# Optimization experiments

Hardware: AMD Instinct MI355X
Metric: run time of the kernel (lower is better)

## Reference

```python
import jax, jax.numpy as jnp
import numpy as np

N_NODES = 100000


def gcn_conv(x, edge_index, W, b, add_self_loops=True):
    """PyG GCNConv: out = D^{-1/2}(A+I)D^{-1/2} (x @ W) + b, sum-aggregated at col."""
    n = x.shape[0]
    x = x @ W  # linear first, like PyG (smaller feature dim usually)
    row, col = edge_index[0], edge_index[1]
    if add_self_loops:
        loop = jnp.arange(n, dtype=row.dtype)
        row = jnp.concatenate([row, loop])
        col = jnp.concatenate([col, loop])
    ones = jnp.ones(row.shape[0], dtype=x.dtype)
    deg = jax.ops.segment_sum(ones, col, num_segments=n)  # in-degree incl. self loops
    dinv = jnp.where(deg > 0, jax.lax.rsqrt(deg), 0.0)
    norm = dinv[row] * dinv[col]  # [E]
    msg = x[row] * norm[:, None]  # gather + scale, [E, F]
    out = jax.ops.segment_sum(msg, col, num_segments=n)  # scatter-add
    return out + b


def setup_inputs() -> dict:
    key = jax.random.key(0)
    ks = jax.random.split(key, 12)
    latent_dim, condition_dim, hidden_dim, output_dim = 64, 32, 64, 64
    n_edges = 1600000
    latent = jax.random.normal(ks[0], (N_NODES, latent_dim), dtype=jnp.float32)
    condition = jax.random.normal(ks[1], (N_NODES, condition_dim), dtype=jnp.float32)
    edge_index = jax.random.randint(ks[2], (2, n_edges), 0, N_NODES, dtype=jnp.int64 if jax.config.jax_enable_x64 else jnp.int32)

    def glorot(k, fan_in, fan_out):
        s = jnp.sqrt(6.0 / (fan_in + fan_out))
        return jax.random.uniform(k, (fan_in, fan_out), minval=-s, maxval=s, dtype=jnp.float32)

    W1 = glorot(ks[3], latent_dim, hidden_dim); b1 = jnp.zeros((hidden_dim,), jnp.float32)
    W2 = glorot(ks[4], condition_dim, hidden_dim); b2 = jnp.zeros((hidden_dim,), jnp.float32)
    W3 = glorot(ks[5], 2 * hidden_dim, hidden_dim); b3 = jnp.zeros((hidden_dim,), jnp.float32)
    W4 = glorot(ks[6], hidden_dim, output_dim); b4 = jnp.zeros((output_dim,), jnp.float32)
    return {"latent": latent, "condition": condition, "edge_index": edge_index,
            "W1": W1, "b1": b1, "W2": W2, "b2": b2,
            "W3": W3, "b3": b3, "W4": W4, "b4": b4}


def reference(latent, condition, edge_index, W1, b1, W2, b2, W3, b3, W4, b4):
    z2h = gcn_conv(latent, edge_index, W1, b1)
    c2h = gcn_conv(condition, edge_index, W2, b2)
    h = jnp.concatenate([z2h, c2h], axis=1)
    h = gcn_conv(h, edge_index, W3, b3)
    out = gcn_conv(h, edge_index, W4, b4)
    return out
```

## Files before the change

kernel.cpp:

```cpp
#include <hip/hip_runtime.h>
#include <hip/hip_fp16.h>

#define BKN 4
#define CBN 256
#define CHUNK 4096
#define MAXBIN 5120

typedef _Float16 half8 __attribute__((ext_vector_type(8)));
typedef float floatx4 __attribute__((ext_vector_type(4)));


__global__ void zero_int_kernel(int* __restrict__ p, int n) {
    int i = blockIdx.x * blockDim.x + threadIdx.x;
    if (i < n) p[i] = 0;
}


__global__ __launch_bounds__(256) void histCB_kernel(const int* __restrict__ ei,
                                                     int* __restrict__ cntCB,
                                                     int E, int NCB) {
    __shared__ int lcnt[512];
    int tid = threadIdx.x;
    for (int i = tid; i < 512; i += 256) lcnt[i] = 0;
    __syncthreads();
    int base = blockIdx.x * CHUNK;
    #pragma unroll
    for (int q = 0; q < 16; ++q) {
        int e = base + q * 256 + tid;
        if (e < E) atomicAdd(&lcnt[ei[E + e] >> 8], 1);
    }
    __syncthreads();
    for (int i = tid; i < NCB; i += 256)
        if (lcnt[i]) atomicAdd(&cntCB[i], lcnt[i]);
}


__global__ __launch_bounds__(512) void scanCB_kernel(const int* __restrict__ cntCB,
                                                     int* __restrict__ offCB,
                                                     int* __restrict__ curCB, int NCB) {
    __shared__ int sA[512], sB[512];
    int tid = threadIdx.x;
    sA[tid] = (tid < NCB) ? cntCB[tid] : 0;
    __syncthreads();
    int* src = sA; int* dst = sB;
    for (int o = 1; o < 512; o <<= 1) {
        dst[tid] = src[tid] + (tid >= o ? src[tid - o] : 0);
        __syncthreads();
        int* t = src; src = dst; dst = t;
    }
    if (tid <= NCB) {
        int v = (tid > 0) ? src[tid - 1] : 0;
        offCB[tid] = v;
        if (tid < NCB) curCB[tid] = v;
    }
}


__global__ __launch_bounds__(256) void passA_kernel(const int* __restrict__ ei,
                                                    int* __restrict__ curCB,
                                                    unsigned* __restrict__ binned,
                                                    int E, int NCB) {
    __shared__ int lcnt[512];
    __shared__ int sA[512], sB[512];
    __shared__ int loffx[512];
    __shared__ int gbase[512];
    __shared__ int lpos[512];
    __shared__ unsigned stage[CHUNK];
    int tid = threadIdx.x;
    int base = blockIdx.x * CHUNK;
    for (int i = tid; i < 512; i += 256) lcnt[i] = 0;
    __syncthreads();
    unsigned pk[16]; int bin[16];
    #pragma unroll
    for (int q = 0; q < 16; ++q) {
        int e = base + q * 256 + tid;
        if (e < E) {
            int r = ei[e], c = ei[E + e];
            pk[q] = ((unsigned)r << 8) | (unsigned)(c & 255);
            bin[q] = c >> 8;
            atomicAdd(&lcnt[bin[q]], 1);
        } else bin[q] = -1;
    }
    __syncthreads();
    for (int i = tid; i < 512; i += 256) sA[i] = lcnt[i];
    __syncthreads();
    int* src = sA; int* dst = sB;
    for (int o = 1; o < 512; o <<= 1) {
        for (int i = tid; i < 512; i += 256)
            dst[i] = src[i] + (i >= o ? src[i - o] : 0);
        __syncthreads();
        int* t = src; src = dst; dst = t;
    }
    for (int i = tid; i < 512; i += 256) {
        int ex = (i > 0) ? src[i - 1] : 0;
        loffx[i] = ex;
        lpos[i] = ex;
        int c = lcnt[i];
        gbase[i] = (c > 0 && i < NCB) ? atomicAdd(&curCB[i], c) : 0;
    }
    __syncthreads();
    #pragma unroll
    for (int q = 0; q < 16; ++q) {
        if (bin[q] >= 0) {
            int p = atomicAdd(&lpos[bin[q]], 1);
            stage[p] = pk[q];
        }
    }
    __syncthreads();
    for (int b = tid; b < NCB; b += 256) {
        int n = lcnt[b];
        int g = gbase[b];
        int lo = loffx[b];
        for (int i2 = 0; i2 < n; ++i2) binned[g + i2] = stage[lo + i2];
    }
}


__global__ __launch_bounds__(256) void passB_kernel(const unsigned* __restrict__ binned,
                                                    const int* __restrict__ offCB,
                                                    unsigned* __restrict__ bkt,
                                                    int* __restrict__ offB,
                                                    float* __restrict__ dinv,
                                                    int N, int NCB, int NB) {
    __shared__ unsigned raw[MAXBIN];
    __shared__ unsigned stage[MAXBIN];
    __shared__ int fcnt[64], foff[65], fpos[64];
    __shared__ int ncnt[256];
    int i = blockIdx.x;
    int tid = threadIdx.x;
    int g0 = offCB[i], g1 = offCB[i + 1];
    int cnt = g1 - g0;
    if (cnt > MAXBIN) cnt = MAXBIN;
    for (int j = tid; j < 64; j += 256) fcnt[j] = 0;
    ncnt[tid] = 0;
    __syncthreads();
    for (int idx = tid; idx < cnt; idx += 256) {
        unsigned pk = binned[g0 + idx];
        raw[idx] = pk;
        atomicAdd(&fcnt[(pk >> 2) & 63], 1);
        atomicAdd(&ncnt[pk & 255], 1);
    }
    __syncthreads();
    if (tid == 0) {
        int run = 0;
        for (int j = 0; j < 64; ++j) { foff[j] = run; run += fcnt[j]; }
        foff[64] = run;
    }
    __syncthreads();
    if (tid < 64) fpos[tid] = foff[tid];
    __syncthreads();
    for (int idx = tid; idx < cnt; idx += 256) {
        unsigned pk = raw[idx];
        int p = atomicAdd(&fpos[(pk >> 2) & 63], 1);
        stage[p] = ((pk >> 8) << 2) | (pk & 3);
    }
    __syncthreads();
    for (int idx = tid; idx < cnt; idx += 256) bkt[g0 + idx] = stage[idx];
    int fb0 = i * 64;
    int nfb = min(64, NB - fb0);
    for (int j = tid; j < nfb; j += 256) offB[fb0 + j] = g0 + foff[j];
    if (i == NCB - 1 && tid == 0) offB[NB] = g1;
    int n0 = i * CBN;
    int n = n0 + tid;
    if (n < N) dinv[n] = rsqrtf((float)ncnt[tid] + 1.0f);
}

__global__ __launch_bounds__(256) void fold_kernel(
    const float* __restrict__ W1, const float* __restrict__ b1,
    const float* __restrict__ W2, const float* __restrict__ b2,
    const float* __restrict__ W3, const float* __restrict__ b3,
    const float* __restrict__ W4,
    float* __restrict__ Wf1, float* __restrict__ Wf2,
    float* __restrict__ u, float* __restrict__ v) {
    __shared__ float As[64][64];
    __shared__ float gsl[64];
    int tid = threadIdx.x;
    int f = tid & 63;
    int w = __builtin_amdgcn_readfirstlane(tid >> 6);
    int blk = blockIdx.x;

    float w4c[64];
    #pragma unroll
    for (int k = 0; k < 64; ++k) w4c[k] = W4[k * 64 + f];

    if (blk < 24) {
        const int half = (blk < 16) ? 0 : 64;
        #pragma unroll 2
        for (int kk = 0; kk < 16; ++kk) {
            int k = w * 16 + kk;
            float a = 0.f;
            #pragma unroll
            for (int j = 0; j < 64; ++j)
                a += W3[(half + k) * 64 + j] * w4c[j];
            As[k][f] = a;
        }
        __syncthreads();
        const float* Wsrc = (blk < 16) ? W1 : W2;
        float* Wdst = (blk < 16) ? Wf1 : Wf2;
        int i = ((blk < 16) ? blk : (blk - 16)) * 4 + w;
        float a = 0.f;
        #pragma unroll
        for (int k = 0; k < 64; ++k)
            a += Wsrc[i * 64 + k] * As[k][f];
        Wdst[i * 64 + f] = a;
    } else {
        float g = 0.f;
        #pragma unroll
        for (int k = 0; k < 64; ++k) g += b1[k] * W3[k * 64 + f];
        #pragma unroll
        for (int k = 0; k < 64; ++k) g += b2[k] * W3[(64 + k) * 64 + f];
        if (w == 0) gsl[f] = g;
        __syncthreads();
        if (w == 0) {
            float uu = 0.f, vv = 0.f;
            #pragma unroll
            for (int k = 0; k < 64; ++k) {
                uu += gsl[k] * w4c[k];
                vv += b3[k] * w4c[k];
            }
            u[f] = uu;
            v[f] = vv;
        }
    }
}

__global__ __launch_bounds__(256) void linZ_kernel(
    const float* __restrict__ lat, const float* __restrict__ cond,
    const float* __restrict__ Wf1, const float* __restrict__ Wf2,
    const float* __restrict__ dinv, _Float16* __restrict__ Z, int N) {
    __shared__ _Float16 Xs[64][104];
    __shared__ _Float16 Wt[64][104];
    int tid = threadIdx.x;
    int n0 = blockIdx.x * 64;
    {
        const float4* lat4 = (const float4*)(lat + (size_t)n0 * 64);
        #pragma unroll
        for (int q = 0; q < 4; ++q) {
            int idx = q * 256 + tid;
            int row = idx >> 4;
            float4 v = make_float4(0.f, 0.f, 0.f, 0.f);
            if (n0 + row < N) v = lat4[idx];
            int col = (idx & 15) * 4;
            Xs[row][col + 0] = (_Float16)v.x;
            Xs[row][col + 1] = (_Float16)v.y;
            Xs[row][col + 2] = (_Float16)v.z;
            Xs[row][col + 3] = (_Float16)v.w;
        }
        const float4* cond4 = (const float4*)(cond + (size_t)n0 * 32);
        #pragma unroll
        for (int q = 0; q < 2; ++q) {
            int idx = q * 256 + tid;
            int row = idx >> 3;
            float4 v = make_float4(0.f, 0.f, 0.f, 0.f);
            if (n0 + row < N) v = cond4[idx];
            int col = 64 + (idx & 7) * 4;
            Xs[row][col + 0] = (_Float16)v.x;
            Xs[row][col + 1] = (_Float16)v.y;
            Xs[row][col + 2] = (_Float16)v.z;
            Xs[row][col + 3] = (_Float16)v.w;
        }
        for (int i = tid; i < 4096; i += 256) {
            int k = i >> 6, f = i & 63;
            Wt[f][k] = (_Float16)Wf1[i];
        }
        for (int i = tid; i < 2048; i += 256) {
            int k = i >> 6, f = i & 63;
            Wt[f][64 + k] = (_Float16)Wf2[i];
        }
    }
    __syncthreads();
    int lane = tid & 63, wave = tid >> 6;
    int quad = lane >> 4, l16 = lane & 15;
    floatx4 acc[4] = {};
    #pragma unroll
    for (int kc = 0; kc < 96; kc += 32) {
        half8 a = *(const half8*)&Xs[wave * 16 + l16][kc + quad * 8];
        #pragma unroll
        for (int nt = 0; nt < 4; ++nt) {
            half8 b = *(const half8*)&Wt[nt * 16 + l16][kc + quad * 8];
            acc[nt] = __builtin_amdgcn_mfma_f32_16x16x32_f16(a, b, acc[nt], 0, 0, 0);
        }
    }
    #pragma unroll
    for (int r = 0; r < 4; ++r) {
        int n = n0 + wave * 16 + quad * 4 + r;
        if (n < N) {
            float d = dinv[n];
            #pragma unroll
            for (int nt = 0; nt < 4; ++nt)
                Z[(size_t)n * 64 + nt * 16 + l16] = (_Float16)(acc[nt][r] * d);
        }
    }
}

template <bool FINAL>
__global__ __launch_bounds__(256) void hop_kernel(
    const _Float16* __restrict__ Vp, const float* __restrict__ dinv,
    const int* __restrict__ offB, const unsigned* __restrict__ bkt,
    const float* __restrict__ wvec, void* __restrict__ outv, int NB) {
    int lane = threadIdx.x & 63;
    int wave = threadIdx.x >> 6;
    int b = blockIdx.x * 4 + wave;
    if (b >= NB) return;
    int c0 = b * BKN;
    float acc0 = (float)Vp[(size_t)(c0 + 0) * 64 + lane];
    float acc1 = (float)Vp[(size_t)(c0 + 1) * 64 + lane];
    float acc2 = (float)Vp[(size_t)(c0 + 2) * 64 + lane];
    float acc3 = (float)Vp[(size_t)(c0 + 3) * 64 + lane];
    int s = offB[b], e = offB[b + 1];
    for (int gb = s; gb < e; gb += 64) {
        int active = min(64, e - gb);
        unsigned pkv = (lane < active) ? bkt[gb + lane] : 0u;
        int k = 0;
        for (; k + 8 <= active; k += 8) {
            unsigned pk0 = __builtin_amdgcn_readlane(pkv, k + 0);
            unsigned pk1 = __builtin_amdgcn_readlane(pkv, k + 1);
            unsigned pk2 = __builtin_amdgcn_readlane(pkv, k + 2);
            unsigned pk3 = __builtin_amdgcn_readlane(pkv, k + 3);
            unsigned pk4 = __builtin_amdgcn_readlane(pkv, k + 4);
            unsigned pk5 = __builtin_amdgcn_readlane(pkv, k + 5);
            unsigned pk6 = __builtin_amdgcn_readlane(pkv, k + 6);
            unsigned pk7 = __builtin_amdgcn_readlane(pkv, k + 7);
            float v0 = (float)Vp[(size_t)(pk0 >> 2) * 64 + lane];
            float v1 = (float)Vp[(size_t)(pk1 >> 2) * 64 + lane];
            float v2 = (float)Vp[(size_t)(pk2 >> 2) * 64 + lane];
            float v3 = (float)Vp[(size_t)(pk3 >> 2) * 64 + lane];
            float v4 = (float)Vp[(size_t)(pk4 >> 2) * 64 + lane];
            float v5 = (float)Vp[(size_t)(pk5 >> 2) * 64 + lane];
            float v6 = (float)Vp[(size_t)(pk6 >> 2) * 64 + lane];
            float v7 = (float)Vp[(size_t)(pk7 >> 2) * 64 + lane];
            int t0 = pk0 & 3, t1 = pk1 & 3, t2 = pk2 & 3, t3 = pk3 & 3;
            int t4 = pk4 & 3, t5 = pk5 & 3, t6 = pk6 & 3, t7 = pk7 & 3;
            acc0 += (t0 == 0) ? v0 : 0.f; acc1 += (t0 == 1) ? v0 : 0.f;
            acc2 += (t0 == 2) ? v0 : 0.f; acc3 += (t0 == 3) ? v0 : 0.f;
            acc0 += (t1 == 0) ? v1 : 0.f; acc1 += (t1 == 1) ? v1 : 0.f;
            acc2 += (t1 == 2) ? v1 : 0.f; acc3 += (t1 == 3) ? v1 : 0.f;
            acc0 += (t2 == 0) ? v2 : 0.f; acc1 += (t2 == 1) ? v2 : 0.f;
            acc2 += (t2 == 2) ? v2 : 0.f; acc3 += (t2 == 3) ? v2 : 0.f;
            acc0 += (t3 == 0) ? v3 : 0.f; acc1 += (t3 == 1) ? v3 : 0.f;
            acc2 += (t3 == 2) ? v3 : 0.f; acc3 += (t3 == 3) ? v3 : 0.f;
            acc0 += (t4 == 0) ? v4 : 0.f; acc1 += (t4 == 1) ? v4 : 0.f;
            acc2 += (t4 == 2) ? v4 : 0.f; acc3 += (t4 == 3) ? v4 : 0.f;
            acc0 += (t5 == 0) ? v5 : 0.f; acc1 += (t5 == 1) ? v5 : 0.f;
            acc2 += (t5 == 2) ? v5 : 0.f; acc3 += (t5 == 3) ? v5 : 0.f;
            acc0 += (t6 == 0) ? v6 : 0.f; acc1 += (t6 == 1) ? v6 : 0.f;
            acc2 += (t6 == 2) ? v6 : 0.f; acc3 += (t6 == 3) ? v6 : 0.f;
            acc0 += (t7 == 0) ? v7 : 0.f; acc1 += (t7 == 1) ? v7 : 0.f;
            acc2 += (t7 == 2) ? v7 : 0.f; acc3 += (t7 == 3) ? v7 : 0.f;
        }
        for (; k + 4 <= active; k += 4) {
            unsigned pk0 = __builtin_amdgcn_readlane(pkv, k + 0);
            unsigned pk1 = __builtin_amdgcn_readlane(pkv, k + 1);
            unsigned pk2 = __builtin_amdgcn_readlane(pkv, k + 2);
            unsigned pk3 = __builtin_amdgcn_readlane(pkv, k + 3);
            float v0 = (float)Vp[(size_t)(pk0 >> 2) * 64 + lane];
            float v1 = (float)Vp[(size_t)(pk1 >> 2) * 64 + lane];
            float v2 = (float)Vp[(size_t)(pk2 >> 2) * 64 + lane];
            float v3 = (float)Vp[(size_t)(pk3 >> 2) * 64 + lane];
            int t0 = pk0 & 3, t1 = pk1 & 3, t2 = pk2 & 3, t3 = pk3 & 3;
            acc0 += (t0 == 0) ? v0 : 0.f; acc1 += (t0 == 1) ? v0 : 0.f;
            acc2 += (t0 == 2) ? v0 : 0.f; acc3 += (t0 == 3) ? v0 : 0.f;
            acc0 += (t1 == 0) ? v1 : 0.f; acc1 += (t1 == 1) ? v1 : 0.f;
            acc2 += (t1 == 2) ? v1 : 0.f; acc3 += (t1 == 3) ? v1 : 0.f;
            acc0 += (t2 == 0) ? v2 : 0.f; acc1 += (t2 == 1) ? v2 : 0.f;
            acc2 += (t2 == 2) ? v2 : 0.f; acc3 += (t2 == 3) ? v2 : 0.f;
            acc0 += (t3 == 0) ? v3 : 0.f; acc1 += (t3 == 1) ? v3 : 0.f;
            acc2 += (t3 == 2) ? v3 : 0.f; acc3 += (t3 == 3) ? v3 : 0.f;
        }
        for (; k < active; ++k) {
            unsigned pk = __builtin_amdgcn_readlane(pkv, k);
            float v = (float)Vp[(size_t)(pk >> 2) * 64 + lane];
            int t = pk & 3;
            acc0 += (t == 0) ? v : 0.f; acc1 += (t == 1) ? v : 0.f;
            acc2 += (t == 2) ? v : 0.f; acc3 += (t == 3) ? v : 0.f;
        }
    }
    float d0 = dinv[c0 + 0], d1 = dinv[c0 + 1], d2 = dinv[c0 + 2], d3 = dinv[c0 + 3];
    float wv = wvec[lane];
    if constexpr (FINAL) {
        float* out = (float*)outv;
        out[(size_t)(c0 + 0) * 64 + lane] = acc0 * d0 + wv;
        out[(size_t)(c0 + 1) * 64 + lane] = acc1 * d1 + wv;
        out[(size_t)(c0 + 2) * 64 + lane] = acc2 * d2 + wv;
        out[(size_t)(c0 + 3) * 64 + lane] = acc3 * d3 + wv;
    } else {
        _Float16* out = (_Float16*)outv;
        out[(size_t)(c0 + 0) * 64 + lane] = (_Float16)(acc0 * d0 * d0 + d0 * wv);
        out[(size_t)(c0 + 1) * 64 + lane] = (_Float16)(acc1 * d1 * d1 + d1 * wv);
        out[(size_t)(c0 + 2) * 64 + lane] = (_Float16)(acc2 * d2 * d2 + d2 * wv);
        out[(size_t)(c0 + 3) * 64 + lane] = (_Float16)(acc3 * d3 * d3 + d3 * wv);
    }
}


static inline size_t align256(size_t x) { return (x + 255) & ~(size_t)255; }

extern "C" void kernel_launch(void* const* d_in, const int* in_sizes, int n_in,
                              void* d_out, int out_size, void* d_ws, size_t ws_size,
                              hipStream_t stream) {
    const float* latent = (const float*)d_in[0];
    const float* cond   = (const float*)d_in[1];
    const int*   ei     = (const int*)d_in[2];
    const float* W1 = (const float*)d_in[3];
    const float* b1 = (const float*)d_in[4];
    const float* W2 = (const float*)d_in[5];
    const float* b2 = (const float*)d_in[6];
    const float* W3 = (const float*)d_in[7];
    const float* b3 = (const float*)d_in[8];
    const float* W4 = (const float*)d_in[9];
    const float* b4 = (const float*)d_in[10];
    float* out = (float*)d_out;

    const int N = in_sizes[0] / 64;
    const int E = in_sizes[2] / 2;
    const int NB  = (N + BKN - 1) / BKN;
    const int NCB = (N + CBN - 1) / CBN;
    const int NCH = (E + CHUNK - 1) / CHUNK;

    char* w = (char*)d_ws;
    size_t o = 0;
    int* cntCB = (int*)(w + o); o = align256(o + (size_t)NCB * 4);
    int* offCB = (int*)(w + o); o = align256(o + (size_t)(NCB + 1) * 4);
    int* curCB = (int*)(w + o); o = align256(o + (size_t)NCB * 4);
    int* offB  = (int*)(w + o); o = align256(o + (size_t)(NB + 1) * 4);
    float* dinv = (float*)(w + o); o = align256(o + (size_t)N * 4);
    float* Wf1 = (float*)(w + o); o = align256(o + 4096 * 4);
    float* Wf2 = (float*)(w + o); o = align256(o + 2048 * 4);
    float* uVec = (float*)(w + o); o = align256(o + 64 * 4);
    float* vVec = (float*)(w + o); o = align256(o + 64 * 4);
    unsigned* binned = (unsigned*)(w + o); o = align256(o + (size_t)E * 4);
    unsigned* bkt    = (unsigned*)(w + o); o = align256(o + (size_t)E * 4);
    _Float16* Z = (_Float16*)(w + o); o = align256(o + (size_t)N * 64 * 2);
    _Float16* P = (_Float16*)(w + o); o = align256(o + (size_t)N * 64 * 2);

    const int BS = 256;
    int gHop = (NB + 3) / 4;

    zero_int_kernel<<<2, BS, 0, stream>>>(cntCB, NCB);
    histCB_kernel<<<NCH, BS, 0, stream>>>(ei, cntCB, E, NCB);
    scanCB_kernel<<<1, 512, 0, stream>>>(cntCB, offCB, curCB, NCB);
    passA_kernel<<<NCH, BS, 0, stream>>>(ei, curCB, binned, E, NCB);
    passB_kernel<<<NCB, BS, 0, stream>>>(binned, offCB, bkt, offB, dinv, N, NCB, NB);

    fold_kernel<<<25, BS, 0, stream>>>(W1, b1, W2, b2, W3, b3, W4, Wf1, Wf2, uVec, vVec);
    linZ_kernel<<<(N + 63) / 64, BS, 0, stream>>>(latent, cond, Wf1, Wf2, dinv, Z, N);

    hop_kernel<false><<<gHop, BS, 0, stream>>>(Z, dinv, offB, bkt, uVec, (void*)P, NB);
    hop_kernel<false><<<gHop, BS, 0, stream>>>(P, dinv, offB, bkt, vVec, (void*)Z, NB);
    hop_kernel<true ><<<gHop, BS, 0, stream>>>(Z, dinv, offB, bkt, b4, (void*)out, NB);
}
```

Before: 316.5 us.

## Process four edges per wave with vectorized 8-byte feature gathers in hop kernel

The hop kernel's wave is split into four 16-lane groups. Each group handles a different edge at once and loads 4 half features per lane as one 8-byte vector, instead of every lane loading one half per edge. Partial sums are combined across groups with xor shuffles, and outputs are written with vector stores. This is meant to raise memory-level parallelism and cut per-edge instruction and scalar readlane overhead. In exchange it adds 16 accumulators per lane, extra FMAs with select masks, and a shuffle reduction at the end.

```diff
diff --git a/kernel.cpp b/kernel.cpp
--- a/kernel.cpp
+++ b/kernel.cpp
@@ -7,6 +7,7 @@
 #define MAXBIN 5120
 
 typedef _Float16 half8 __attribute__((ext_vector_type(8)));
+typedef _Float16 h4v __attribute__((ext_vector_type(4)));
 typedef float floatx4 __attribute__((ext_vector_type(4)));
 
 
@@ -302,93 +303,74 @@
     int wave = threadIdx.x >> 6;
     int b = blockIdx.x * 4 + wave;
     if (b >= NB) return;
+    int g  = lane >> 4;
+    int fq = lane & 15;
     int c0 = b * BKN;
-    float acc0 = (float)Vp[(size_t)(c0 + 0) * 64 + lane];
-    float acc1 = (float)Vp[(size_t)(c0 + 1) * 64 + lane];
-    float acc2 = (float)Vp[(size_t)(c0 + 2) * 64 + lane];
-    float acc3 = (float)Vp[(size_t)(c0 + 3) * 64 + lane];
+
+    float acc[4][4];
+    {
+        h4v h = *(const h4v*)&Vp[(size_t)(c0 + g) * 64 + fq * 4];
+        #pragma unroll
+        for (int t = 0; t < 4; ++t)
+            #pragma unroll
+            for (int j = 0; j < 4; ++j)
+                acc[t][j] = (t == g) ? (float)h[j] : 0.f;
+    }
+
     int s = offB[b], e = offB[b + 1];
-    for (int gb = s; gb < e; gb += 64) {
-        int active = min(64, e - gb);
-        unsigned pkv = (lane < active) ? bkt[gb + lane] : 0u;
-        int k = 0;
-        for (; k + 8 <= active; k += 8) {
-            unsigned pk0 = __builtin_amdgcn_readlane(pkv, k + 0);
-            unsigned pk1 = __builtin_amdgcn_readlane(pkv, k + 1);
-            unsigned pk2 = __builtin_amdgcn_readlane(pkv, k + 2);
-            unsigned pk3 = __builtin_amdgcn_readlane(pkv, k + 3);
-            unsigned pk4 = __builtin_amdgcn_readlane(pkv, k + 4);
-            unsigned pk5 = __builtin_amdgcn_readlane(pkv, k + 5);
-            unsigned pk6 = __builtin_amdgcn_readlane(pkv, k + 6);
-            unsigned pk7 = __builtin_amdgcn_readlane(pkv, k + 7);
-            float v0 = (float)Vp[(size_t)(pk0 >> 2) * 64 + lane];
-            float v1 = (float)Vp[(size_t)(pk1 >> 2) * 64 + lane];
-            float v2 = (float)Vp[(size_t)(pk2 >> 2) * 64 + lane];
-            float v3 = (float)Vp[(size_t)(pk3 >> 2) * 64 + lane];
-            float v4 = (float)Vp[(size_t)(pk4 >> 2) * 64 + lane];
-            float v5 = (float)Vp[(size_t)(pk5 >> 2) * 64 + lane];
-            float v6 = (float)Vp[(size_t)(pk6 >> 2) * 64 + lane];
-            float v7 = (float)Vp[(size_t)(pk7 >> 2) * 64 + lane];
-            int t0 = pk0 & 3, t1 = pk1 & 3, t2 = pk2 & 3, t3 = pk3 & 3;
-            int t4 = pk4 & 3, t5 = pk5 & 3, t6 = pk6 & 3, t7 = pk7 & 3;
-            acc0 += (t0 == 0) ? v0 : 0.f; acc1 += (t0 == 1) ? v0 : 0.f;
-            acc2 += (t0 == 2) ? v0 : 0.f; acc3 += (t0 == 3) ? v0 : 0.f;
-            acc0 += (t1 == 0) ? v1 : 0.f; acc1 += (t1 == 1) ? v1 : 0.f;
-            acc2 += (t1 == 2) ? v1 : 0.f; acc3 += (t1 == 3) ? v1 : 0.f;
-            acc0 += (t2 == 0) ? v2 : 0.f; acc1 += (t2 == 1) ? v2 : 0.f;
-            acc2 += (t2 == 2) ? v2 : 0.f; acc3 += (t2 == 3) ? v2 : 0.f;
-            acc0 += (t3 == 0) ? v3 : 0.f; acc1 += (t3 == 1) ? v3 : 0.f;
-            acc2 += (t3 == 2) ? v3 : 0.f; acc3 += (t3 == 3) ? v3 : 0.f;
-            acc0 += (t4 == 0) ? v4 : 0.f; acc1 += (t4 == 1) ? v4 : 0.f;
-            acc2 += (t4 == 2) ? v4 : 0.f; acc3 += (t4 == 3) ? v4 : 0.f;
-            acc0 += (t5 == 0) ? v5 : 0.f; acc1 += (t5 == 1) ? v5 : 0.f;
-            acc2 += (t5 == 2) ? v5 : 0.f; acc3 += (t5 == 3) ? v5 : 0.f;
-            acc0 += (t6 == 0) ? v6 : 0.f; acc1 += (t6 == 1) ? v6 : 0.f;
-            acc2 += (t6 == 2) ? v6 : 0.f; acc3 += (t6 == 3) ? v6 : 0.f;
-            acc0 += (t7 == 0) ? v7 : 0.f; acc1 += (t7 == 1) ? v7 : 0.f;
-            acc2 += (t7 == 2) ? v7 : 0.f; acc3 += (t7 == 3) ? v7 : 0.f;
-        }
-        for (; k + 4 <= active; k += 4) {
-            unsigned pk0 = __builtin_amdgcn_readlane(pkv, k + 0);
-            unsigned pk1 = __builtin_amdgcn_readlane(pkv, k + 1);
-            unsigned pk2 = __builtin_amdgcn_readlane(pkv, k + 2);
-            unsigned pk3 = __builtin_amdgcn_readlane(pkv, k + 3);
-            float v0 = (float)Vp[(size_t)(pk0 >> 2) * 64 + lane];
-            float v1 = (float)Vp[(size_t)(pk1 >> 2) * 64 + lane];
-            float v2 = (float)Vp[(size_t)(pk2 >> 2) * 64 + lane];
-            float v3 = (float)Vp[(size_t)(pk3 >> 2) * 64 + lane];
-            int t0 = pk0 & 3, t1 = pk1 & 3, t2 = pk2 & 3, t3 = pk3 & 3;
-            acc0 += (t0 == 0) ? v0 : 0.f; acc1 += (t0 == 1) ? v0 : 0.f;
-            acc2 += (t0 == 2) ? v0 : 0.f; acc3 += (t0 == 3) ? v0 : 0.f;
-            acc0 += (t1 == 0) ? v1 : 0.f; acc1 += (t1 == 1) ? v1 : 0.f;
-            acc2 += (t1 == 2) ? v1 : 0.f; acc3 += (t1 == 3) ? v1 : 0.f;
-            acc0 += (t2 == 0) ? v2 : 0.f; acc1 += (t2 == 1) ? v2 : 0.f;
-            acc2 += (t2 == 2) ? v2 : 0.f; acc3 += (t2 == 3) ? v2 : 0.f;
-            acc0 += (t3 == 0) ? v3 : 0.f; acc1 += (t3 == 1) ? v3 : 0.f;
-            acc2 += (t3 == 2) ? v3 : 0.f; acc3 += (t3 == 3) ? v3 : 0.f;
-        }
-        for (; k < active; ++k) {
-            unsigned pk = __builtin_amdgcn_readlane(pkv, k);
-            float v = (float)Vp[(size_t)(pk >> 2) * 64 + lane];
-            int t = pk & 3;
-            acc0 += (t == 0) ? v : 0.f; acc1 += (t == 1) ? v : 0.f;
-            acc2 += (t == 2) ? v : 0.f; acc3 += (t == 3) ? v : 0.f;
-        }
-    }
-    float d0 = dinv[c0 + 0], d1 = dinv[c0 + 1], d2 = dinv[c0 + 2], d3 = dinv[c0 + 3];
-    float wv = wvec[lane];
+    #pragma unroll 4
+    for (int i0 = s; i0 < e; i0 += 4) {
+        int idx = i0 + g;
+        unsigned pk = bkt[min(idx, e - 1)];
+        int te = (idx < e) ? (int)(pk & 3u) : 4;
+        int r  = (int)(pk >> 2);
+        h4v h = *(const h4v*)&Vp[(size_t)r * 64 + fq * 4];
+        float v0 = (float)h[0], v1 = (float)h[1];
+        float v2 = (float)h[2], v3 = (float)h[3];
+        #pragma unroll
+        for (int t = 0; t < 4; ++t) {
+            float sel = (te == t) ? 1.f : 0.f;
+            acc[t][0] = fmaf(sel, v0, acc[t][0]);
+            acc[t][1] = fmaf(sel, v1, acc[t][1]);
+            acc[t][2] = fmaf(sel, v2, acc[t][2]);
+            acc[t][3] = fmaf(sel, v3, acc[t][3]);
+        }
+    }
+
+    #pragma unroll
+    for (int t = 0; t < 4; ++t)
+        #pragma unroll
+        for (int j = 0; j < 4; ++j) {
+            float x = acc[t][j];
+            x += __shfl_xor(x, 16, 64);
+            x += __shfl_xor(x, 32, 64);
+            acc[t][j] = x;
+        }
+
+    float og[4];
+    #pragma unroll
+    for (int j = 0; j < 4; ++j) {
+        float x0 = (g == 0) ? acc[0][j] : acc[1][j];
+        float x1 = (g == 2) ? acc[2][j] : acc[3][j];
+        og[j] = (g < 2) ? x0 : x1;
+    }
+    float d = dinv[c0 + g];
+    float4 wv = *(const float4*)&wvec[fq * 4];
     if constexpr (FINAL) {
-        float* out = (float*)outv;
-        out[(size_t)(c0 + 0) * 64 + lane] = acc0 * d0 + wv;
-        out[(size_t)(c0 + 1) * 64 + lane] = acc1 * d1 + wv;
-        out[(size_t)(c0 + 2) * 64 + lane] = acc2 * d2 + wv;
-        out[(size_t)(c0 + 3) * 64 + lane] = acc3 * d3 + wv;
+        float4 o;
+        o.x = og[0] * d + wv.x;
+        o.y = og[1] * d + wv.y;
+        o.z = og[2] * d + wv.z;
+        o.w = og[3] * d + wv.w;
+        *(float4*)&((float*)outv)[(size_t)(c0 + g) * 64 + fq * 4] = o;
     } else {
-        _Float16* out = (_Float16*)outv;
-        out[(size_t)(c0 + 0) * 64 + lane] = (_Float16)(acc0 * d0 * d0 + d0 * wv);
-        out[(size_t)(c0 + 1) * 64 + lane] = (_Float16)(acc1 * d1 * d1 + d1 * wv);
-        out[(size_t)(c0 + 2) * 64 + lane] = (_Float16)(acc2 * d2 * d2 + d2 * wv);
-        out[(size_t)(c0 + 3) * 64 + lane] = (_Float16)(acc3 * d3 * d3 + d3 * wv);
+        float dd = d * d;
+        h4v o;
+        o[0] = (_Float16)(og[0] * dd + d * wv.x);
+        o[1] = (_Float16)(og[1] * dd + d * wv.y);
+        o[2] = (_Float16)(og[2] * dd + d * wv.z);
+        o[3] = (_Float16)(og[3] * dd + d * wv.w);
+        *(h4v*)&((_Float16*)outv)[(size_t)(c0 + g) * 64 + fq * 4] = o;
     }
 }
 
```

Result: faster. 277.7 us (-12.3%).
